# Performance work log

Measured on AMD Instinct MI355X. Metric: run time of the kernel, lower is better.

## Reference

```python
import jax, jax.numpy as jnp
import numpy as np

N, A, B, K = 100000, 64, 128, 27  # active sites, in/out channels, 3^3 offsets
EPS = 1e-4  # scn BatchNorm default eps
LEAK = 0.0  # leakiness=0 -> ReLU


def bn_lrelu(x, gamma, beta):
    # training-mode BN over active sites, fused leaky relu
    mu = x.mean(0)
    var = x.var(0)
    xh = (x - mu) * jax.lax.rsqrt(var + EPS) * gamma + beta
    return jnp.where(xh > 0, xh, LEAK * xh)


def subconv(f, nbr, mask, W):
    # submanifold conv via rulebook: f [N,Cin], nbr [N,K], mask [N,K], W [K,Cin,Cout]
    out = jnp.zeros((f.shape[0], W.shape[2]), f.dtype)
    for k in range(W.shape[0]):  # fixed small set of kernel offsets
        g = jnp.where(mask[:, k:k + 1], f[nbr[:, k]], jnp.zeros((), f.dtype))
        out = out + g @ W[k]
    return out


def setup_inputs() -> dict:
    key = jax.random.key(0)
    ks = jax.random.split(key, 8)
    feat = jax.random.normal(ks[0], (N, A), jnp.float32)
    nbr = jax.random.randint(ks[1], (N, K), 0, N, jnp.int32)
    mask = jax.random.randint(ks[2], (N, K), 0, 2, jnp.int32).astype(bool)
    # self-connection at center offset is always valid in submanifold conv
    center = K // 2
    nbr = nbr.at[:, center].set(jnp.arange(N, dtype=jnp.int32))
    mask = mask.at[:, center].set(True)
    s1 = 1.0 / np.sqrt(K * A)
    s2 = 1.0 / np.sqrt(K * B)
    W1 = jax.random.normal(ks[3], (K, A, B), jnp.float32) * s1
    W2 = jax.random.normal(ks[4], (K, B, B), jnp.float32) * s2
    Wnin = jax.random.normal(ks[5], (A, B), jnp.float32) / np.sqrt(A)
    gamma1 = jnp.ones((A,), jnp.float32)
    beta1 = jnp.zeros((A,), jnp.float32)
    gamma2 = jnp.ones((B,), jnp.float32)
    beta2 = jnp.zeros((B,), jnp.float32)
    return {"feat": feat, "gamma1": gamma1, "beta1": beta1, "W1": W1,
            "gamma2": gamma2, "beta2": beta2, "W2": W2, "Wnin": Wnin,
            "nbr": nbr, "mask": mask}


def reference(feat, gamma1, beta1, W1, gamma2, beta2, W2, Wnin, nbr, mask):
    y1 = feat @ Wnin  # NetworkInNetwork shortcut (a != b)
    h = bn_lrelu(feat, gamma1, beta1)
    h = subconv(h, nbr, mask, W1)
    h = bn_lrelu(h, gamma2, beta2)
    y2 = subconv(h, nbr, mask, W2)
    return y1 + y2  # add_feature_planes
```

## Files before the change

kernel.cpp:

```cpp
#include <hip/hip_runtime.h>
#include <stdint.h>

#define CA 64
#define CB 128
#define KOFF 27
#define BN_EPS 1e-4f

typedef short bf16x8 __attribute__((ext_vector_type(8)));
typedef float f32x4 __attribute__((ext_vector_type(4)));
typedef unsigned int u32x4 __attribute__((ext_vector_type(4)));
typedef unsigned short u16x4 __attribute__((ext_vector_type(4)));

__device__ __forceinline__ unsigned short f2bf(float f) {
  union { float f; uint32_t u; } c; c.f = f;
  uint32_t u = c.u;
  return (unsigned short)((u + 0x7FFFu + ((u >> 16) & 1u)) >> 16);
}

__global__ void detect_mask_k(const unsigned char* __restrict__ m, int* flag) {
  unsigned v = 0;
  for (int i = threadIdx.x; i < 4096; i += 256)
    if (i & 3) v |= m[i];
  if (v) atomicOr(flag, 1);
}

__global__ void pack_mask_k(const void* __restrict__ mp, const int* __restrict__ flag,
                            uint32_t* __restrict__ bits, int n) {
  int i = blockIdx.x * blockDim.x + threadIdx.x;
  if (i >= n) return;
  uint32_t b = 0;
  if (*flag) {
    const unsigned char* m = (const unsigned char*)mp + (size_t)i * KOFF;
    for (int k = 0; k < KOFF; k++) b |= (m[k] ? 1u : 0u) << k;
  } else {
    const int* m = (const int*)mp + (size_t)i * KOFF;
    for (int k = 0; k < KOFF; k++) b |= (m[k] ? 1u : 0u) << k;
  }
  bits[i] = b;
}

__global__ void transpose_all_k(const float* __restrict__ W1, const float* __restrict__ W2,
                                const float* __restrict__ Wnin,
                                unsigned short* __restrict__ w1t, unsigned short* __restrict__ w2t,
                                unsigned short* __restrict__ wnt) {
  const int t1 = KOFF * CA * CB, t2 = KOFF * CB * CB, t3 = CA * CB;
  int idx = blockIdx.x * blockDim.x + threadIdx.x;
  if (idx < t1) {
    int ci = idx % CA; int r = idx / CA; int co = r % CB; int k = r / CB;
    w1t[idx] = f2bf(W1[((size_t)k * CA + ci) * CB + co]);
  } else if (idx < t1 + t2) {
    int j = idx - t1;
    int ci = j % CB; int r = j / CB; int co = r % CB; int k = r / CB;
    w2t[j] = f2bf(W2[((size_t)k * CB + ci) * CB + co]);
  } else if (idx < t1 + t2 + t3) {
    int j = idx - t1 - t2;
    int ci = j % CA; int co = j / CA;
    wnt[j] = f2bf(Wnin[(size_t)ci * CB + co]);
  }
}

template<int C>
__global__ void col_stats_k(const float* __restrict__ x, int n, float* __restrict__ sums) {
  __shared__ float ssum[C], ssq[C];
  int t = threadIdx.x;
  for (int i = t; i < C; i += 256) { ssum[i] = 0.f; ssq[i] = 0.f; }
  __syncthreads();
  const int c = t % C;
  const int rpb = 256 / C;
  float s = 0.f, q = 0.f;
  for (int r = blockIdx.x * rpb + t / C; r < n; r += gridDim.x * rpb) {
    float v = x[(size_t)r * C + c];
    s += v; q += v * v;
  }
  atomicAdd(&ssum[c], s);
  atomicAdd(&ssq[c], q);
  __syncthreads();
  for (int i = t; i < C; i += 256) {
    atomicAdd(&sums[i], ssum[i]);
    atomicAdd(&sums[C + i], ssq[i]);
  }
}

template<int C>
__global__ void bn_finalize_k(const float* __restrict__ sums, const float* __restrict__ gamma,
                              const float* __restrict__ beta, float* __restrict__ sc, int n) {
  int c = threadIdx.x;
  if (c >= C) return;
  float inv_n = 1.f / (float)n;
  float mean = sums[c] * inv_n;
  float var = sums[C + c] * inv_n - mean * mean;
  float rstd = rsqrtf(var + BN_EPS);
  float scale = gamma[c] * rstd;
  sc[c] = scale;
  sc[C + c] = beta[c] - mean * scale;
}

template<int C, bool RAW>
__global__ void bn_apply_k(const float* __restrict__ x, const float* __restrict__ sc,
                           unsigned short* __restrict__ h, unsigned short* __restrict__ raw,
                           int total) {
  int idx = (blockIdx.x * blockDim.x + threadIdx.x) * 4;
  if (idx >= total) return;
  f32x4 v = *(const f32x4*)&x[idx];
  int c0 = idx % C;
  u16x4 ho, ro;
#pragma unroll
  for (int j = 0; j < 4; j++) {
    float s = sc[c0 + j], b = sc[C + c0 + j];
    float hv = fmaxf(v[j] * s + b, 0.f);
    ho[j] = f2bf(hv);
    if (RAW) ro[j] = f2bf(v[j]);
  }
  *(u16x4*)&h[idx] = ho;
  if (RAW) *(u16x4*)&raw[idx] = ro;
}

template<int CIN, bool FUSE, bool STATS>
__launch_bounds__(256)
__global__ void conv_k(const unsigned short* __restrict__ hin,
                       const unsigned short* __restrict__ wt,
                       const int* __restrict__ nbr,
                       const uint32_t* __restrict__ mbits,
                       const unsigned short* __restrict__ fbraw,
                       const unsigned short* __restrict__ wnt,
                       const char* __restrict__ zpage,
                       float* __restrict__ out, float* __restrict__ sums, int n) {
  constexpr int TR = 64;
  constexpr int NKS = CIN / 32;
  constexpr int CH = CIN / 8;
  constexpr int RPP = 256 / CH;
  constexpr int RPW = 64 / CH;
  constexpr int NP = TR / RPP;

  __shared__ alignas(16) unsigned short tile[2][TR * CIN];

  const int t = threadIdx.x;
  const int lane = t & 63;
  const int wave = t >> 6;
  const int l16 = lane & 15;
  const int quad = lane >> 4;
  const int colbase = wave * 32;
  const int rowbase = blockIdx.x * TR;
  const int nrows = min(TR, n - rowbase);

  const int c16 = t % CH;
  const int grow = t / CH;
  const char* hsrc = (const char*)hin + (c16 ^ (grow & (CH - 1))) * 16;
  const int wvrow = wave * RPW;

  uint32_t pm[NP]; int nbro[NP];
#pragma unroll
  for (int p = 0; p < NP; p++) {
    int rg = rowbase + p * RPP + grow;
    pm[p] = (rg < n) ? mbits[rg] : 0u;
    nbro[p] = min(rg, n - 1) * KOFF;
  }

  const int boff0 = (colbase + l16) * CIN + quad * 8;
  const int boff1 = boff0 + 16 * CIN;

  f32x4 acc[4][2];
#pragma unroll
  for (int i = 0; i < 4; i++) { acc[i][0] = f32x4{0,0,0,0}; acc[i][1] = f32x4{0,0,0,0}; }

  bf16x8 bfr[2 * NKS];
  int nbE[NP], nbO[NP];

#define NBLOAD(kk, nb)                                                         \
  { _Pragma("unroll")                                                          \
    for (int p = 0; p < NP; p++) nb[p] = nbr[nbro[p] + (kk)]; }

#define DMASTAGE(kk, buf, nb)                                                  \
  { _Pragma("unroll")                                                          \
    for (int p = 0; p < NP; p++) {                                             \
      const char* g = ((pm[p] >> (kk)) & 1u)                                   \
          ? hsrc + (size_t)((unsigned)nb[p] * (unsigned)(CIN * 2))             \
          : zpage;                                                             \
      __builtin_amdgcn_global_load_lds(                                        \
          (const __attribute__((address_space(1))) void*)g,                    \
          (__attribute__((address_space(3))) void*)                            \
              &tile[buf][(p * RPP + wvrow) * CIN],                             \
          16, 0, 0);                                                           \
    } }

#define LOADB(kk, dst)                                                         \
  {                                                                            \
    const unsigned short* wk = wt + (size_t)(kk) * (CB * CIN);                 \
    _Pragma("unroll")                                                          \
    for (int ks = 0; ks < NKS; ks++) {                                         \
      dst[2 * ks]     = *(const bf16x8*)&wk[boff0 + ks * 32];                  \
      dst[2 * ks + 1] = *(const bf16x8*)&wk[boff1 + ks * 32];                  \
    }                                                                          \
  }

#define MMA(buf)                                                               \
  {                                                                            \
    _Pragma("unroll")                                                          \
    for (int ks = 0; ks < NKS; ks++) {                                         \
      _Pragma("unroll")                                                        \
      for (int rt = 0; rt < 4; rt++) {                                         \
        int row = rt * 16 + l16;                                               \
        bf16x8 a = *(const bf16x8*)&tile[buf][row * CIN +                      \
                      (((ks * 4 + quad) ^ (row & (CH - 1))) * 8)];             \
        acc[rt][0] = __builtin_amdgcn_mfma_f32_16x16x32_bf16(a, bfr[2 * ks],     acc[rt][0], 0, 0, 0); \
        acc[rt][1] = __builtin_amdgcn_mfma_f32_16x16x32_bf16(a, bfr[2 * ks + 1], acc[rt][1], 0, 0, 0); \
      }                                                                        \
    }                                                                          \
  }

#define WAITBAR()                                                              \
  asm volatile("s_waitcnt vmcnt(%0) lgkmcnt(0)\n\ts_barrier"                   \
               :: "i"(2 * NKS) : "memory")

  NBLOAD(0, nbE);
  DMASTAGE(0, 0, nbE);
  NBLOAD(1, nbO);
  __builtin_amdgcn_sched_barrier(0);

  if constexpr (FUSE) {
#pragma unroll
    for (int ks = 0; ks < CA / 32; ks++) {
      bf16x8 b0 = *(const bf16x8*)&wnt[(colbase + l16) * CA + ks * 32 + quad * 8];
      bf16x8 b1 = *(const bf16x8*)&wnt[(colbase + 16 + l16) * CA + ks * 32 + quad * 8];
#pragma unroll
      for (int rt = 0; rt < 4; rt++) {
        int r = rt * 16 + l16;
        bf16x8 a = bf16x8{0, 0, 0, 0, 0, 0, 0, 0};
        if (r < nrows)
          a = *(const bf16x8*)&fbraw[(size_t)(rowbase + r) * CA + ks * 32 + quad * 8];
        acc[rt][0] = __builtin_amdgcn_mfma_f32_16x16x32_bf16(a, b0, acc[rt][0], 0, 0, 0);
        acc[rt][1] = __builtin_amdgcn_mfma_f32_16x16x32_bf16(a, b1, acc[rt][1], 0, 0, 0);
      }
    }
  }

  LOADB(0, bfr);
  WAITBAR();

#pragma unroll
  for (int k = 0; k < KOFF; k++) {
    const int cur = k & 1, nxt = cur ^ 1;
    if (k + 1 < KOFF) {
      if (((k + 1) & 1) == 0) DMASTAGE(k + 1, nxt, nbE) else DMASTAGE(k + 1, nxt, nbO);
      if (k + 2 < KOFF) {
        if (((k + 2) & 1) == 0) NBLOAD(k + 2, nbE) else NBLOAD(k + 2, nbO);
      }
      __builtin_amdgcn_sched_barrier(0);
    }
    MMA(cur);
    if (k + 1 < KOFF) {
      LOADB(k + 1, bfr);
      WAITBAR();
    }
  }
#undef NBLOAD
#undef DMASTAGE
#undef LOADB
#undef MMA
#undef WAITBAR

#pragma unroll
  for (int rt = 0; rt < 4; rt++) {
#pragma unroll
    for (int ct = 0; ct < 2; ct++) {
#pragma unroll
      for (int i = 0; i < 4; i++) {
        int r = rt * 16 + quad * 4 + i;
        if (r < nrows) {
          int c = colbase + ct * 16 + l16;
          out[(size_t)(rowbase + r) * CB + c] = acc[rt][ct][i];
        }
      }
    }
  }

  if constexpr (STATS) {
#pragma unroll
    for (int ct = 0; ct < 2; ct++) {
      float s = 0.f, q = 0.f;
#pragma unroll
      for (int rt = 0; rt < 4; rt++)
#pragma unroll
        for (int i = 0; i < 4; i++) { float v = acc[rt][ct][i]; s += v; q += v * v; }
      s += __shfl_xor(s, 16); s += __shfl_xor(s, 32);
      q += __shfl_xor(q, 16); q += __shfl_xor(q, 32);
      if (quad == 0) {
        int cch = colbase + ct * 16 + l16;
        atomicAdd(&sums[cch], s);
        atomicAdd(&sums[CB + cch], q);
      }
    }
  }
}

extern "C" void kernel_launch(void* const* d_in, const int* in_sizes, int n_in,
                              void* d_out, int out_size, void* d_ws, size_t ws_size,
                              hipStream_t stream) {
  const float* feat   = (const float*)d_in[0];
  const float* gamma1 = (const float*)d_in[1];
  const float* beta1  = (const float*)d_in[2];
  const float* W1     = (const float*)d_in[3];
  const float* gamma2 = (const float*)d_in[4];
  const float* beta2  = (const float*)d_in[5];
  const float* W2     = (const float*)d_in[6];
  const float* Wnin   = (const float*)d_in[7];
  const int*   nbr    = (const int*)d_in[8];
  const void*  mask   = d_in[9];
  float* out = (float*)d_out;

  const int n = in_sizes[0] / CA;

  char* ws = (char*)d_ws;
  size_t off = 0;
  auto alloc = [&](size_t bytes) { size_t p = off; off += (bytes + 255) & ~(size_t)255; return p; };
  int*            flag  = (int*)           (ws + alloc(256));
  char*           zpage = (char*)          (ws + alloc(256));
  float*          sums1 = (float*)         (ws + alloc(2 * CA * 4));
  float*          sums2 = (float*)         (ws + alloc(2 * CB * 4));
  float*          sc1   = (float*)         (ws + alloc(2 * CA * 4));
  float*          sc2   = (float*)         (ws + alloc(2 * CB * 4));
  uint32_t*       mbits = (uint32_t*)      (ws + alloc((size_t)n * 4));
  unsigned short* fb    = (unsigned short*)(ws + alloc((size_t)n * CA * 2));
  unsigned short* hb1   = (unsigned short*)(ws + alloc((size_t)n * CA * 2));
  float*          out1  = (float*)         (ws + alloc((size_t)n * CB * 4));
  unsigned short* hb2   = (unsigned short*)(ws + alloc((size_t)n * CB * 2));
  unsigned short* w1t   = (unsigned short*)(ws + alloc((size_t)KOFF * CB * CA * 2));
  unsigned short* w2t   = (unsigned short*)(ws + alloc((size_t)KOFF * CB * CB * 2));
  unsigned short* wnt   = (unsigned short*)(ws + alloc((size_t)CB * CA * 2));

  hipMemsetAsync(d_ws, 0, 2048, stream);

  detect_mask_k<<<1, 256, 0, stream>>>((const unsigned char*)mask, flag);
  pack_mask_k<<<(n + 255) / 256, 256, 0, stream>>>(mask, flag, mbits, n);

  {
    int tot = KOFF * CA * CB + KOFF * CB * CB + CA * CB;
    transpose_all_k<<<(tot + 255) / 256, 256, 0, stream>>>(W1, W2, Wnin, w1t, w2t, wnt);
  }

  col_stats_k<CA><<<256, 256, 0, stream>>>(feat, n, sums1);
  bn_finalize_k<CA><<<1, CA, 0, stream>>>(sums1, gamma1, beta1, sc1, n);
  bn_apply_k<CA, true><<<(n * CA / 4 + 255) / 256, 256, 0, stream>>>(feat, sc1, hb1, fb, n * CA);

  conv_k<CA, false, true><<<(n + 63) / 64, 256, 0, stream>>>(hb1, w1t, nbr, mbits, nullptr, nullptr, zpage, out1, sums2, n);

  bn_finalize_k<CB><<<1, CB, 0, stream>>>(sums2, gamma2, beta2, sc2, n);
  bn_apply_k<CB, false><<<(n * CB / 4 + 255) / 256, 256, 0, stream>>>(out1, sc2, hb2, nullptr, n * CB);

  conv_k<CB, true, false><<<(n + 63) / 64, 256, 0, stream>>>(hb2, w2t, nbr, mbits, fb, wnt, zpage, out, nullptr, n);
}
```

Baseline: 513.7 us.

## Deepen conv gather pipeline to triple-buffered LDS with double-buffered weights

The gather tile buffer goes from two to three LDS stages, so the DMA for offset k+2 is issued while offset k is computed. Neighbor indices are prefetched four offsets ahead, and the weight fragments are double-buffered and loaded one offset ahead. The wait counts are retuned so each barrier waits only for the stage about to be consumed. This is meant to hide gather latency better, at the cost of more LDS per block and more registers, which may lower occupancy.

```diff
diff --git a/kernel.cpp b/kernel.cpp
--- a/kernel.cpp
+++ b/kernel.cpp
@@ -132,7 +132,7 @@
   constexpr int RPW = 64 / CH;
   constexpr int NP = TR / RPP;
 
-  __shared__ alignas(16) unsigned short tile[2][TR * CIN];
+  __shared__ alignas(16) unsigned short tile[3][TR * CIN];
 
   const int t = threadIdx.x;
   const int lane = t & 63;
@@ -163,14 +163,19 @@
 #pragma unroll
   for (int i = 0; i < 4; i++) { acc[i][0] = f32x4{0,0,0,0}; acc[i][1] = f32x4{0,0,0,0}; }
 
-  bf16x8 bfr[2 * NKS];
-  int nbE[NP], nbO[NP];
-
-#define NBLOAD(kk, nb)                                                         \
+  bf16x8 bfrE[2 * NKS], bfrO[2 * NKS];
+  int nb0[NP], nb1[NP], nb2[NP];
+
+#define NBLS(kk, nb)                                                           \
   { _Pragma("unroll")                                                          \
     for (int p = 0; p < NP; p++) nb[p] = nbr[nbro[p] + (kk)]; }
-
-#define DMASTAGE(kk, buf, nb)                                                  \
+#define NBL(kk) do {                                                           \
+    if (((kk) % 3) == 0)      NBLS(kk, nb0)                                    \
+    else if (((kk) % 3) == 1) NBLS(kk, nb1)                                    \
+    else                      NBLS(kk, nb2)                                    \
+  } while (0)
+
+#define DMAS(kk, bi, nb)                                                       \
   { _Pragma("unroll")                                                          \
     for (int p = 0; p < NP; p++) {                                             \
       const char* g = ((pm[p] >> (kk)) & 1u)                                   \
@@ -179,9 +184,14 @@
       __builtin_amdgcn_global_load_lds(                                        \
           (const __attribute__((address_space(1))) void*)g,                    \
           (__attribute__((address_space(3))) void*)                            \
-              &tile[buf][(p * RPP + wvrow) * CIN],                             \
+              &tile[bi][(p * RPP + wvrow) * CIN],                              \
           16, 0, 0);                                                           \
     } }
+#define DMAD(kk) do {                                                          \
+    if (((kk) % 3) == 0)      DMAS(kk, 0, nb0)                                 \
+    else if (((kk) % 3) == 1) DMAS(kk, 1, nb1)                                 \
+    else                      DMAS(kk, 2, nb2)                                 \
+  } while (0)
 
 #define LOADB(kk, dst)                                                         \
   {                                                                            \
@@ -192,30 +202,37 @@
       dst[2 * ks + 1] = *(const bf16x8*)&wk[boff1 + ks * 32];                  \
     }                                                                          \
   }
-
-#define MMA(buf)                                                               \
+#define LOADBD(kk) do {                                                        \
+    if (((kk) & 1) == 0) LOADB(kk, bfrE) else LOADB(kk, bfrO)                  \
+  } while (0)
+
+#define MMA(bi, bn)                                                            \
   {                                                                            \
     _Pragma("unroll")                                                          \
     for (int ks = 0; ks < NKS; ks++) {                                         \
       _Pragma("unroll")                                                        \
       for (int rt = 0; rt < 4; rt++) {                                         \
         int row = rt * 16 + l16;                                               \
-        bf16x8 a = *(const bf16x8*)&tile[buf][row * CIN +                      \
+        bf16x8 a = *(const bf16x8*)&tile[bi][row * CIN +                       \
                       (((ks * 4 + quad) ^ (row & (CH - 1))) * 8)];             \
-        acc[rt][0] = __builtin_amdgcn_mfma_f32_16x16x32_bf16(a, bfr[2 * ks],     acc[rt][0], 0, 0, 0); \
-        acc[rt][1] = __builtin_amdgcn_mfma_f32_16x16x32_bf16(a, bfr[2 * ks + 1], acc[rt][1], 0, 0, 0); \
+        acc[rt][0] = __builtin_amdgcn_mfma_f32_16x16x32_bf16(a, bn[2 * ks],     acc[rt][0], 0, 0, 0); \
+        acc[rt][1] = __builtin_amdgcn_mfma_f32_16x16x32_bf16(a, bn[2 * ks + 1], acc[rt][1], 0, 0, 0); \
       }                                                                        \
     }                                                                          \
   }
-
-#define WAITBAR()                                                              \
+#define MMAD(k_) do {                                                          \
+    if (((k_) % 3) == 0)      { if (((k_) & 1) == 0) MMA(0, bfrE) else MMA(0, bfrO) } \
+    else if (((k_) % 3) == 1) { if (((k_) & 1) == 0) MMA(1, bfrE) else MMA(1, bfrO) } \
+    else                      { if (((k_) & 1) == 0) MMA(2, bfrE) else MMA(2, bfrO) } \
+  } while (0)
+
+#define WAITBAR(keep)                                                          \
   asm volatile("s_waitcnt vmcnt(%0) lgkmcnt(0)\n\ts_barrier"                   \
-               :: "i"(2 * NKS) : "memory")
-
-  NBLOAD(0, nbE);
-  DMASTAGE(0, 0, nbE);
-  NBLOAD(1, nbO);
-  __builtin_amdgcn_sched_barrier(0);
+               :: "i"(keep) : "memory")
+
+  NBL(0); NBL(1); NBL(2);
+  DMAD(0);
+  NBL(3);
 
   if constexpr (FUSE) {
 #pragma unroll
@@ -234,29 +251,33 @@
     }
   }
 
-  LOADB(0, bfr);
-  WAITBAR();
+  LOADBD(0);
+  __builtin_amdgcn_sched_barrier(0);
+  DMAD(1);
+  WAITBAR(NP);
 
 #pragma unroll
   for (int k = 0; k < KOFF; k++) {
-    const int cur = k & 1, nxt = cur ^ 1;
     if (k + 1 < KOFF) {
-      if (((k + 1) & 1) == 0) DMASTAGE(k + 1, nxt, nbE) else DMASTAGE(k + 1, nxt, nbO);
-      if (k + 2 < KOFF) {
-        if (((k + 2) & 1) == 0) NBLOAD(k + 2, nbE) else NBLOAD(k + 2, nbO);
-      }
+      LOADBD(k + 1);
       __builtin_amdgcn_sched_barrier(0);
     }
-    MMA(cur);
+    if (k + 2 < KOFF) DMAD(k + 2);
+    if (k + 4 < KOFF) NBL(k + 4);
+    __builtin_amdgcn_sched_barrier(0);
+    MMAD(k);
     if (k + 1 < KOFF) {
-      LOADB(k + 1, bfr);
-      WAITBAR();
-    }
-  }
-#undef NBLOAD
-#undef DMASTAGE
+      WAITBAR(((k + 2 < KOFF) ? NP : 0) + ((k + 4 < KOFF) ? NP : 0) + 2 * NKS);
+    }
+  }
+#undef NBLS
+#undef NBL
+#undef DMAS
+#undef DMAD
 #undef LOADB
+#undef LOADBD
 #undef MMA
+#undef MMAD
 #undef WAITBAR
 
 #pragma unroll
```

Measured after the change: 506.3 us. Within noise of the previous version (-1.4%).

## Use 8 waves per conv block with 16 output columns each

Applied to the files above, without the earlier changes.

Each conv block now runs 512 threads (8 waves), and each wave computes 16 output columns instead of 32. This halves per-wave accumulator and B-fragment registers and spreads the gather DMA staging across more threads. The B fragments are double-buffered in even/odd register sets so the next offset's weights can load while the current MMA runs. The trade-off is that each A fragment read from LDS feeds only one MFMA, so LDS read traffic per FLOP doubles, and barriers now synchronize twice as many waves.

```diff
diff --git a/kernel.cpp b/kernel.cpp
--- a/kernel.cpp
+++ b/kernel.cpp
@@ -116,7 +116,7 @@
 }
 
 template<int CIN, bool FUSE, bool STATS>
-__launch_bounds__(256)
+__launch_bounds__(512)
 __global__ void conv_k(const unsigned short* __restrict__ hin,
                        const unsigned short* __restrict__ wt,
                        const int* __restrict__ nbr,
@@ -128,7 +128,7 @@
   constexpr int TR = 64;
   constexpr int NKS = CIN / 32;
   constexpr int CH = CIN / 8;
-  constexpr int RPP = 256 / CH;
+  constexpr int RPP = 512 / CH;
   constexpr int RPW = 64 / CH;
   constexpr int NP = TR / RPP;
 
@@ -139,7 +139,7 @@
   const int wave = t >> 6;
   const int l16 = lane & 15;
   const int quad = lane >> 4;
-  const int colbase = wave * 32;
+  const int colbase = wave * 16;
   const int rowbase = blockIdx.x * TR;
   const int nrows = min(TR, n - rowbase);
 
@@ -156,14 +156,13 @@
     nbro[p] = min(rg, n - 1) * KOFF;
   }
 
-  const int boff0 = (colbase + l16) * CIN + quad * 8;
-  const int boff1 = boff0 + 16 * CIN;
-
-  f32x4 acc[4][2];
-#pragma unroll
-  for (int i = 0; i < 4; i++) { acc[i][0] = f32x4{0,0,0,0}; acc[i][1] = f32x4{0,0,0,0}; }
-
-  bf16x8 bfr[2 * NKS];
+  const int boff = (colbase + l16) * CIN + quad * 8;
+
+  f32x4 acc[4];
+#pragma unroll
+  for (int i = 0; i < 4; i++) acc[i] = f32x4{0, 0, 0, 0};
+
+  bf16x8 bfrE[NKS], bfrO[NKS];
   int nbE[NP], nbO[NP];
 
 #define NBLOAD(kk, nb)                                                         \
@@ -187,13 +186,11 @@
   {                                                                            \
     const unsigned short* wk = wt + (size_t)(kk) * (CB * CIN);                 \
     _Pragma("unroll")                                                          \
-    for (int ks = 0; ks < NKS; ks++) {                                         \
-      dst[2 * ks]     = *(const bf16x8*)&wk[boff0 + ks * 32];                  \
-      dst[2 * ks + 1] = *(const bf16x8*)&wk[boff1 + ks * 32];                  \
-    }                                                                          \
-  }
-
-#define MMA(buf)                                                               \
+    for (int ks = 0; ks < NKS; ks++)                                           \
+      dst[ks] = *(const bf16x8*)&wk[boff + ks * 32];                           \
+  }
+
+#define MMA(buf, bn)                                                           \
   {                                                                            \
     _Pragma("unroll")                                                          \
     for (int ks = 0; ks < NKS; ks++) {                                         \
@@ -202,15 +199,14 @@
         int row = rt * 16 + l16;                                               \
         bf16x8 a = *(const bf16x8*)&tile[buf][row * CIN +                      \
                       (((ks * 4 + quad) ^ (row & (CH - 1))) * 8)];             \
-        acc[rt][0] = __builtin_amdgcn_mfma_f32_16x16x32_bf16(a, bfr[2 * ks],     acc[rt][0], 0, 0, 0); \
-        acc[rt][1] = __builtin_amdgcn_mfma_f32_16x16x32_bf16(a, bfr[2 * ks + 1], acc[rt][1], 0, 0, 0); \
+        acc[rt] = __builtin_amdgcn_mfma_f32_16x16x32_bf16(a, bn[ks], acc[rt], 0, 0, 0); \
       }                                                                        \
     }                                                                          \
   }
 
 #define WAITBAR()                                                              \
   asm volatile("s_waitcnt vmcnt(%0) lgkmcnt(0)\n\ts_barrier"                   \
-               :: "i"(2 * NKS) : "memory")
+               :: "i"(NKS) : "memory")
 
   NBLOAD(0, nbE);
   DMASTAGE(0, 0, nbE);
@@ -220,21 +216,19 @@
   if constexpr (FUSE) {
 #pragma unroll
     for (int ks = 0; ks < CA / 32; ks++) {
-      bf16x8 b0 = *(const bf16x8*)&wnt[(colbase + l16) * CA + ks * 32 + quad * 8];
-      bf16x8 b1 = *(const bf16x8*)&wnt[(colbase + 16 + l16) * CA + ks * 32 + quad * 8];
+      bf16x8 b = *(const bf16x8*)&wnt[(colbase + l16) * CA + ks * 32 + quad * 8];
 #pragma unroll
       for (int rt = 0; rt < 4; rt++) {
         int r = rt * 16 + l16;
         bf16x8 a = bf16x8{0, 0, 0, 0, 0, 0, 0, 0};
         if (r < nrows)
           a = *(const bf16x8*)&fbraw[(size_t)(rowbase + r) * CA + ks * 32 + quad * 8];
-        acc[rt][0] = __builtin_amdgcn_mfma_f32_16x16x32_bf16(a, b0, acc[rt][0], 0, 0, 0);
-        acc[rt][1] = __builtin_amdgcn_mfma_f32_16x16x32_bf16(a, b1, acc[rt][1], 0, 0, 0);
+        acc[rt] = __builtin_amdgcn_mfma_f32_16x16x32_bf16(a, b, acc[rt], 0, 0, 0);
       }
     }
   }
 
-  LOADB(0, bfr);
+  LOADB(0, bfrE);
   WAITBAR();
 
 #pragma unroll
@@ -247,9 +241,9 @@
       }
       __builtin_amdgcn_sched_barrier(0);
     }
-    MMA(cur);
+    if ((k & 1) == 0) MMA(0, bfrE) else MMA(1, bfrO);
     if (k + 1 < KOFF) {
-      LOADB(k + 1, bfr);
+      if (((k + 1) & 1) == 0) LOADB(k + 1, bfrE) else LOADB(k + 1, bfrO);
       WAITBAR();
     }
   }
@@ -262,33 +256,27 @@
 #pragma unroll
   for (int rt = 0; rt < 4; rt++) {
 #pragma unroll
-    for (int ct = 0; ct < 2; ct++) {
-#pragma unroll
-      for (int i = 0; i < 4; i++) {
-        int r = rt * 16 + quad * 4 + i;
-        if (r < nrows) {
-          int c = colbase + ct * 16 + l16;
-          out[(size_t)(rowbase + r) * CB + c] = acc[rt][ct][i];
-        }
+    for (int i = 0; i < 4; i++) {
+      int r = rt * 16 + quad * 4 + i;
+      if (r < nrows) {
+        int c = colbase + l16;
+        out[(size_t)(rowbase + r) * CB + c] = acc[rt][i];
       }
     }
   }
 
   if constexpr (STATS) {
-#pragma unroll
-    for (int ct = 0; ct < 2; ct++) {
-      float s = 0.f, q = 0.f;
-#pragma unroll
-      for (int rt = 0; rt < 4; rt++)
-#pragma unroll
-        for (int i = 0; i < 4; i++) { float v = acc[rt][ct][i]; s += v; q += v * v; }
-      s += __shfl_xor(s, 16); s += __shfl_xor(s, 32);
-      q += __shfl_xor(q, 16); q += __shfl_xor(q, 32);
-      if (quad == 0) {
-        int cch = colbase + ct * 16 + l16;
-        atomicAdd(&sums[cch], s);
-        atomicAdd(&sums[CB + cch], q);
-      }
+    float s = 0.f, q = 0.f;
+#pragma unroll
+    for (int rt = 0; rt < 4; rt++)
+#pragma unroll
+      for (int i = 0; i < 4; i++) { float v = acc[rt][i]; s += v; q += v * v; }
+    s += __shfl_xor(s, 16); s += __shfl_xor(s, 32);
+    q += __shfl_xor(q, 16); q += __shfl_xor(q, 32);
+    if (quad == 0) {
+      int cch = colbase + l16;
+      atomicAdd(&sums[cch], s);
+      atomicAdd(&sums[CB + cch], q);
     }
   }
 }
@@ -342,10 +330,10 @@
   bn_finalize_k<CA><<<1, CA, 0, stream>>>(sums1, gamma1, beta1, sc1, n);
   bn_apply_k<CA, true><<<(n * CA / 4 + 255) / 256, 256, 0, stream>>>(feat, sc1, hb1, fb, n * CA);
 
-  conv_k<CA, false, true><<<(n + 63) / 64, 256, 0, stream>>>(hb1, w1t, nbr, mbits, nullptr, nullptr, zpage, out1, sums2, n);
+  conv_k<CA, false, true><<<(n + 63) / 64, 512, 0, stream>>>(hb1, w1t, nbr, mbits, nullptr, nullptr, zpage, out1, sums2, n);
 
   bn_finalize_k<CB><<<1, CB, 0, stream>>>(sums2, gamma2, beta2, sc2, n);
   bn_apply_k<CB, false><<<(n * CB / 4 + 255) / 256, 256, 0, stream>>>(out1, sc2, hb2, nullptr, n * CB);
 
-  conv_k<CB, true, false><<<(n + 63) / 64, 256, 0, stream>>>(hb2, w2t, nbr, mbits, fb, wnt, zpage, out, nullptr, n);
-}
+  conv_k<CB, true, false><<<(n + 63) / 64, 512, 0, stream>>>(hb2, w2t, nbr, mbits, fb, wnt, zpage, out, nullptr, n);
+}
```

Result: no change. 504.1 us (-1.9%).
